# Kernel optimization log

Hardware: AMD Instinct MI355X
Metric: run time of the kernel (lower is better)

The kernel has to match this reference:

```python
import jax, jax.numpy as jnp
import numpy as np

B, T, D, H = 2, 2048, 1024, 16
DK = D // H
NEG = -1e9  # stand-in for -inf; causal mask guarantees >=1 valid key per row


def setup_inputs() -> dict:
    key = jax.random.key(0)
    ks = jax.random.split(key, 9)
    s = 1.0 / np.sqrt(D)
    x = jax.random.normal(ks[0], (B, T, D), dtype=jnp.float32)
    mask = jnp.broadcast_to(jnp.tril(jnp.ones((T, T), dtype=jnp.int32))[None, None], (B, 1, T, T))
    params = {}
    for i, n in enumerate(['q', 'k', 'v', 'o']):
        params['W' + n] = jax.random.normal(ks[1 + 2 * i], (D, D), dtype=jnp.float32) * s
        params['b' + n] = jax.random.normal(ks[2 + 2 * i], (D,), dtype=jnp.float32) * s
    return dict(x=x, mask=mask, **params)


def reference(x, mask, Wq, bq, Wk, bk, Wv, bv, Wo, bo):
    Bx, Tx, Dx = x.shape
    # projections: [B,T,D] -> [B,H,T,DK]
    def split_heads(y):
        return y.reshape(Bx, Tx, H, DK).transpose(0, 2, 1, 3)
    Q = split_heads(x @ Wq + bq)
    K = split_heads(x @ Wk + bk)
    V = split_heads(x @ Wv + bv)
    scores = jnp.einsum('bhqd,bhkd->bhqk', Q, K) / jnp.sqrt(jnp.float32(DK))
    scores = jnp.where(mask == 0, NEG, scores)
    attn = jax.nn.softmax(scores, axis=-1)  # dropout is identity in eval / p=0
    out = jnp.einsum('bhqk,bhkd->bhqd', attn, V)
    out = out.transpose(0, 2, 1, 3).reshape(Bx, Tx, Dx)
    return out @ Wo + bo
```

## Files before the change

kernel.cpp:

```cpp
#include <hip/hip_runtime.h>
#include <hip/hip_bf16.h>

typedef __bf16 bf16;
typedef __attribute__((ext_vector_type(8))) __bf16 bf16x8;
typedef __attribute__((ext_vector_type(4))) __bf16 bf16x4;
typedef __attribute__((ext_vector_type(4))) float f32x4;
typedef __attribute__((ext_vector_type(16))) float f32x16;
typedef __attribute__((ext_vector_type(4))) int int4v;

#define TSEQ 2048
#define DMODEL 1024
#define NHEAD 16
#define DKH 64
#define BATCH 2
#define NQKV 3072

typedef __attribute__((address_space(1))) const void gv_t;
typedef __attribute__((address_space(3))) void sv_t;
__device__ __forceinline__ void gll16(const bf16* g, bf16* s) {
    __builtin_amdgcn_global_load_lds((gv_t*)g, (sv_t*)s, 16, 0, 0);
}
#define WAIT_VM(n) __builtin_amdgcn_s_waitcnt(0x0F70 | (n))

__device__ __forceinline__ unsigned cvtpk(float lo, float hi) {
    unsigned d;
    asm("v_cvt_pk_bf16_f32 %0, %1, %2" : "=v"(d) : "v"(lo), "v"(hi));
    return d;
}

#define PREP_CONV 4096
#define PREP_TW   4096
#define PREP_GRID (PREP_CONV + PREP_TW + 12)
__global__ __launch_bounds__(256) void prep(
    const float* __restrict__ x,
    const float* __restrict__ Wq, const float* __restrict__ Wk,
    const float* __restrict__ Wv, const float* __restrict__ Wo,
    const float* __restrict__ bq, const float* __restrict__ bk,
    const float* __restrict__ bv,
    bf16* __restrict__ xb, bf16* __restrict__ WT, float* __restrict__ biasO)
{
    __shared__ float t[32][33];
    int bid = blockIdx.x;
    const int tid = threadIdx.x;
    if (bid < PREP_CONV) {
        int i = (bid * 256 + tid) * 4;
        f32x4 v = *(const f32x4*)(x + i);
        bf16x4 o;
#pragma unroll
        for (int j = 0; j < 4; ++j) o[j] = (bf16)v[j];
        *(bf16x4*)(xb + i) = o;
        return;
    }
    bid -= PREP_CONV;
    if (bid < PREP_TW) {
        int z = bid >> 10;
        int by = ((bid >> 5) & 31) * 32, bx = (bid & 31) * 32;
        const float* W = z == 0 ? Wq : z == 1 ? Wk : z == 2 ? Wv : Wo;
        bf16* T = WT + (size_t)z * DMODEL * DMODEL;
        int tx = tid & 31, ty = tid >> 5;
#pragma unroll
        for (int i = 0; i < 4; ++i)
            t[ty + i * 8][tx] = W[(size_t)(by + ty + i * 8) * DMODEL + bx + tx];
        __syncthreads();
#pragma unroll
        for (int i = 0; i < 4; ++i)
            T[(size_t)(bx + ty + i * 8) * DMODEL + by + tx] = (bf16)t[tx][ty + i * 8];
        return;
    }
    bid -= PREP_TW;
    int i = bid * 256 + tid;
    float v = i < 1024 ? bq[i] : i < 2048 ? bk[i - 1024] : bv[i - 2048];
    biasO[i] = v;
}

template <typename OutT, int NW_N, bool FUSE_VT>
__global__ __launch_bounds__(256) void gemm_bias_kernel(
    const bf16* __restrict__ A, const bf16* __restrict__ BT,
    const float* __restrict__ bias, OutT* __restrict__ C, int ldc,
    bf16* __restrict__ VT)
{
    constexpr int BN    = NW_N * 64;
    constexpr int MW    = 4 / NW_N;
    constexpr int WROWS = 128 / MW;
    constexpr int FM    = WROWS / 16;
    constexpr int BK    = 64;
    constexpr int ASZ   = 128 * BK;
    constexpr int BSZ   = BN * BK;
    constexpr int BNP   = BN + 4;
    constexpr int TST   = 136;
    constexpr int EPI   = sizeof(OutT) == 2 ? (FUSE_VT ? 128 * TST : 128 * BN)
                                            : 64 * BNP * 2;
    constexpr int STG   = 2 * ASZ + 2 * BSZ;
    constexpr int SMEM  = STG > EPI ? STG : EPI;
    __shared__ bf16 smem[SMEM];
    bf16* As0 = smem;
    bf16* Bs0 = smem + 2 * ASZ;

    const int tid = threadIdx.x;
    const int ln = tid & 63, wave = tid >> 6;
    const int wm = NW_N == 2 ? (wave >> 1) : wave;
    const int wn = NW_N == 2 ? (wave & 1) : 0;
    const int lr = ln & 15, quad = ln >> 4;

    constexpr int NBX = (NW_N == 2) ? 24 : 16;
    constexpr int CH  = (NW_N == 2) ? 96 : 64;
    const int wg  = blockIdx.x;
    const int lin = (wg & 7) * CH + (wg >> 3);
    const int m0  = (lin / NBX) * 128, n0 = (lin % NBX) * BN;

    f32x4 acc[FM][4] = {};

    const int srow = ln >> 3;
    const int scol = ((ln & 7) ^ srow) * 8;
    const bf16* Ag = A + (size_t)(m0 + wave * 32 + srow) * DMODEL + scol;
    const bf16* Bg = BT + (size_t)(n0 + (NW_N == 2 ? wave * 32 : wave * 16) + srow) * DMODEL + scol;

    auto stage = [&](int buf, int kk) {
        bf16* AsW = As0 + buf * ASZ + wave * (32 * BK);
#pragma unroll
        for (int l = 0; l < 4; ++l)
            gll16(Ag + (size_t)(l * 8) * DMODEL + kk, AsW + l * 8 * BK);
        if constexpr (NW_N == 2) {
            bf16* BsW = Bs0 + buf * BSZ + wave * (32 * BK);
#pragma unroll
            for (int l = 0; l < 4; ++l)
                gll16(Bg + (size_t)(l * 8) * DMODEL + kk, BsW + l * 8 * BK);
        } else {
            bf16* BsW = Bs0 + buf * BSZ + wave * (16 * BK);
#pragma unroll
            for (int l = 0; l < 2; ++l)
                gll16(Bg + (size_t)(l * 8) * DMODEL + kk, BsW + l * 8 * BK);
        }
    };

    constexpr int NT = DMODEL / BK;
    stage(0, 0);
    WAIT_VM(0);
    __syncthreads();
    const int swr = lr & 7;
    for (int kt = 0; kt < NT; ++kt) {
        if (kt + 1 < NT) stage((kt + 1) & 1, (kt + 1) * BK);
        const bf16* AsB = As0 + (kt & 1) * ASZ;
        const bf16* BsB = Bs0 + (kt & 1) * BSZ;
#pragma unroll
        for (int k2 = 0; k2 < 2; ++k2) {
            bf16x8 af[FM], bfr[4];
#pragma unroll
            for (int i = 0; i < FM; ++i)
                af[i] = *(const bf16x8*)(AsB + (wm * WROWS + i * 16 + lr) * BK +
                                         (((k2 * 4 + quad) ^ swr) * 8));
#pragma unroll
            for (int j = 0; j < 4; ++j)
                bfr[j] = *(const bf16x8*)(BsB + (wn * 64 + j * 16 + lr) * BK +
                                          (((k2 * 4 + quad) ^ swr) * 8));
#pragma unroll
            for (int i = 0; i < FM; ++i)
#pragma unroll
                for (int j = 0; j < 4; ++j)
                    acc[i][j] = __builtin_amdgcn_mfma_f32_16x16x32_bf16(
                        af[i], bfr[j], acc[i][j], 0, 0, 0);
        }
        WAIT_VM(0);
        __syncthreads();
    }

    if constexpr (sizeof(OutT) == 2) {
        if (FUSE_VT && n0 >= 2048) {
            bf16* Cs = smem;
#pragma unroll
            for (int j = 0; j < 4; ++j) {
                int nl = wn * 64 + j * 16 + lr;
                float bv = bias[n0 + nl];
#pragma unroll
                for (int i = 0; i < FM; ++i) {
                    int ml = wm * WROWS + i * 16 + quad * 4;
#pragma unroll
                    for (int r = 0; r < 4; ++r)
                        Cs[nl * TST + ml + r] = (bf16)(acc[i][j][r] + bv);
                }
            }
            __syncthreads();
            const int bb = m0 >> 11;
            const int tloc = m0 & 2047;
#pragma unroll
            for (int pp = 0; pp < 8; ++pp) {
                int dl = pp * 16 + (tid >> 4);
                int t0 = (tid & 15) * 8;
                bf16x8 v = *(const bf16x8*)(Cs + dl * TST + t0);
                *(bf16x8*)(VT + (size_t)(bb * 1024 + (n0 - 2048) + dl) * TSEQ +
                           tloc + t0) = v;
            }
            return;
        }
        bf16* Cs = smem;
#pragma unroll
        for (int j = 0; j < 4; ++j) {
            int nl = wn * 64 + j * 16 + lr;
            float bv = bias[n0 + nl];
#pragma unroll
            for (int i = 0; i < FM; ++i) {
                int ml = wm * WROWS + i * 16 + quad * 4;
#pragma unroll
                for (int r = 0; r < 4; ++r)
                    Cs[(ml + r) * BN + nl] = (bf16)(acc[i][j][r] + bv);
            }
        }
        __syncthreads();
        constexpr int LPR = BN / 8;
        constexpr int RPP = 256 / LPR;
        const int rr = tid / LPR, cc = (tid % LPR) * 8;
#pragma unroll
        for (int pp = 0; pp < 128 / RPP; ++pp) {
            int row = pp * RPP + rr;
            *(bf16x8*)(C + (size_t)(m0 + row) * ldc + n0 + cc) =
                *(const bf16x8*)(Cs + row * BN + cc);
        }
    } else {
        float* Cf = (float*)smem;
#pragma unroll
        for (int half = 0; half < 2; ++half) {
            if (((wm * WROWS) >> 6) == half) {
#pragma unroll
                for (int j = 0; j < 4; ++j) {
                    int nl = wn * 64 + j * 16 + lr;
                    float bv = bias[n0 + nl];
#pragma unroll
                    for (int i = 0; i < FM; ++i) {
                        int ml = wm * WROWS + i * 16 + quad * 4 - half * 64;
#pragma unroll
                        for (int r = 0; r < 4; ++r)
                            Cf[(ml + r) * BNP + nl] = acc[i][j][r] + bv;
                    }
                }
            }
            __syncthreads();
            constexpr int LPR = BN / 4;
            constexpr int RPP = 256 / LPR;
            const int rr = tid / LPR, cc = (tid % LPR) * 4;
#pragma unroll
            for (int pp = 0; pp < 64 / RPP; ++pp) {
                int row = pp * RPP + rr;
                *(f32x4*)(C + (size_t)(m0 + half * 64 + row) * ldc + n0 + cc) =
                    *(const f32x4*)(Cf + row * BNP + cc);
            }
            __syncthreads();
        }
    }
}

template <int KTN, bool MASKED>
__device__ __forceinline__ void tile_step(
    int kt0, int kc, int qabs,
    const bf16* __restrict__ Ksb, const bf16* __restrict__ Vsb,
    const bf16x8 qf[4], f32x16 oacc[2], float& lrow,
    int ln31, int hi, int sw)
{
    f32x16 st[KTN] = {};
    __builtin_amdgcn_s_setprio(1);
#pragma unroll
    for (int t = 0; t < KTN; ++t)
#pragma unroll
        for (int ks = 0; ks < 4; ++ks) {
            const bf16x8 ka = *(const bf16x8*)(
                Ksb + (ln31 + (kt0 + t) * 32) * 64 + (((2 * ks + hi) ^ sw) * 8));
            st[t] = __builtin_amdgcn_mfma_f32_32x32x16_bf16(ka, qf[ks], st[t], 0, 0, 0);
        }
    __builtin_amdgcn_s_setprio(0);

    const float scale2 = 0.18033688f;
    float rs = 0.f;
#pragma unroll
    for (int t = 0; t < KTN; ++t)
#pragma unroll
        for (int r = 0; r < 16; ++r) {
            float p = exp2f(fmaf(st[t][r], scale2, -24.0f));
            if (MASKED &&
                (kc + (kt0 + t) * 32 + (r & 3) + 8 * (r >> 2) + 4 * hi > qabs))
                p = 0.f;
            rs += p;
            st[t][r] = p;
        }
    rs += __shfl_xor(rs, 32);
    lrow += rs;

    __builtin_amdgcn_s_setprio(1);
#pragma unroll
    for (int t = 0; t < KTN; ++t)
#pragma unroll
        for (int s2 = 0; s2 < 2; ++s2) {
            const int bb = s2 * 8;
            unsigned c01 = cvtpk(st[t][bb + 0], st[t][bb + 1]);
            unsigned c23 = cvtpk(st[t][bb + 2], st[t][bb + 3]);
            unsigned c45 = cvtpk(st[t][bb + 4], st[t][bb + 5]);
            unsigned c67 = cvtpk(st[t][bb + 6], st[t][bb + 7]);
            asm("v_permlane32_swap_b32 %0, %1" : "+v"(c01), "+v"(c45));
            asm("v_permlane32_swap_b32 %0, %1" : "+v"(c23), "+v"(c67));
            int4v pw;
            pw[0] = (int)c01; pw[1] = (int)c23; pw[2] = (int)c45; pw[3] = (int)c67;
            const bf16x8 pa = __builtin_bit_cast(bf16x8, pw);
            const int ksg = (kt0 + t) * 2 + s2;
#pragma unroll
            for (int dblk = 0; dblk < 2; ++dblk) {
                const bf16x8 vb = *(const bf16x8*)(
                    Vsb + (dblk * 32 + ln31) * 64 + (((2 * ksg + hi) ^ sw) * 8));
                oacc[dblk] = __builtin_amdgcn_mfma_f32_32x32x16_bf16(
                    pa, vb, oacc[dblk], 0, 0, 0);
            }
        }
    __builtin_amdgcn_s_setprio(0);
}

__global__ __launch_bounds__(256, 2) void flash_attn(
    const bf16* __restrict__ QKV, const bf16* __restrict__ VT,
    bf16* __restrict__ O)
{
    __shared__ bf16 Ks[4][64 * 64];
    __shared__ bf16 Vs[4][64 * 64];
    const int tid = threadIdx.x;
    const int ln = tid & 63, w = tid >> 6;
    const int ln31 = ln & 31, hi = ln >> 5, sw = ln & 7;
    const int wg = blockIdx.x;
    const int g = wg & 31, p = wg >> 5;
    const int h = g >> 1, b = g & 1;
    const int q0A = p * 64, q0B = (31 - p) * 64;

    const bf16* Qb = QKV + (size_t)b * TSEQ * NQKV + h * DKH;
    const bf16* Kb = Qb + 1024;
    const bf16* VTb = VT + (size_t)(b * NHEAD + h) * DKH * TSEQ;

    const int q1 = (w < 2 ? q0A : q0B) + (w & 1) * 32 + ln31;
    const int q2 = q0B + (w & 1) * 32 + ln31;

    bf16x8 qf1[4], qf2[4];
#pragma unroll
    for (int ks = 0; ks < 4; ++ks) {
        qf1[ks] = *(const bf16x8*)(Qb + (size_t)q1 * NQKV + ks * 16 + hi * 8);
        qf2[ks] = *(const bf16x8*)(Qb + (size_t)q2 * NQKV + ks * 16 + hi * 8);
    }
    WAIT_VM(0);

    const int srow = (w & 1) * 32 + (ln >> 3);
    const int scol = ((ln & 7) ^ ((ln >> 3) & 7)) * 8;
    const bool stK = (w < 2);
    auto stage = [&](int buf, int kc) {
        if (stK) {
            const bf16* g2 = Kb + (size_t)(kc + srow) * NQKV + scol;
            bf16* s = &Ks[buf][(w & 1) * 32 * 64];
#pragma unroll
            for (int l = 0; l < 4; ++l)
                gll16(g2 + (size_t)(l * 8) * NQKV, s + l * 8 * 64);
        } else {
            const bf16* g2 = VTb + (size_t)srow * TSEQ + kc + scol;
            bf16* s = &Vs[buf][(w & 1) * 32 * 64];
#pragma unroll
            for (int l = 0; l < 4; ++l)
                gll16(g2 + (size_t)(l * 8) * TSEQ, s + l * 8 * 64);
        }
    };

    f32x16 oacc1[2] = {}, oacc2[2] = {};
    float l1 = 0.f, l2 = 0.f;

    const int nld = 32 - p;

    auto do_chunk = [&](int c) {
        const int kc = c * 64;
        const bf16* K = Ks[c & 3];
        const bf16* V = Vs[c & 3];
        if (c <= p) {
            if (w < 2 && c == p)
                tile_step<2, true >(0, kc, q1, K, V, qf1, oacc1, l1, ln31, hi, sw);
            else
                tile_step<2, false>(0, kc, q1, K, V, qf1, oacc1, l1, ln31, hi, sw);
        } else {
            const int kt0 = w >> 1;
            if (c == nld - 1)
                tile_step<1, true >(kt0, kc, q2, K, V, qf2, oacc2, l2, ln31, hi, sw);
            else
                tile_step<1, false>(kt0, kc, q2, K, V, qf2, oacc2, l2, ln31, hi, sw);
        }
    };

    stage(0, 0);
    stage(1, 64);
    for (int c = 0; c < nld; c += 2) {
        WAIT_VM(0);
        __syncthreads();
        if (c + 2 < nld) stage((c + 2) & 3, (c + 2) * 64);
        if (c + 3 < nld) stage((c + 3) & 3, (c + 3) * 64);
        do_chunk(c);
        if (c + 1 < nld) do_chunk(c + 1);
    }
    __syncthreads();

    float* exO = (float*)&Ks[0][0];
    float* exL = (float*)&Vs[0][0];
    if (w < 2) {
        float* dst = exO + w * 2048;
#pragma unroll
        for (int dblk = 0; dblk < 2; ++dblk)
#pragma unroll
            for (int r = 0; r < 16; ++r) {
                int q = (r & 3) + 8 * (r >> 2) + 4 * hi;
                dst[q * 64 + dblk * 32 + ln31] = oacc2[dblk][r];
            }
        if (ln < 32) exL[w * 32 + ln] = l2;
    }
    __syncthreads();

    f32x16 oat[2];
    float lt;
    int qs;
    if (w < 2) {
        oat[0] = oacc1[0]; oat[1] = oacc1[1];
        lt = l1;
        qs = q0A + (w & 1) * 32;
    } else {
        const float* src = exO + (w - 2) * 2048;
        lt = l1 + l2 + exL[(w - 2) * 32 + ln31];
#pragma unroll
        for (int dblk = 0; dblk < 2; ++dblk)
#pragma unroll
            for (int r = 0; r < 16; ++r) {
                int q = (r & 3) + 8 * (r >> 2) + 4 * hi;
                oat[dblk][r] = oacc1[dblk][r] + oacc2[dblk][r] +
                               src[q * 64 + dblk * 32 + ln31];
            }
        qs = q0B + (w & 1) * 32;
    }

#pragma unroll
    for (int r = 0; r < 16; ++r) {
        const int crow = (r & 3) + 8 * (r >> 2) + 4 * hi;
        const float inv = 1.0f / __shfl(lt, crow);
        const int row = qs + crow;
#pragma unroll
        for (int dblk = 0; dblk < 2; ++dblk)
            O[(size_t)(b * TSEQ + row) * DMODEL + h * DKH + dblk * 32 + ln31] =
                (bf16)(oat[dblk][r] * inv);
    }
}

extern "C" void kernel_launch(void* const* d_in, const int* in_sizes, int n_in,
                              void* d_out, int out_size, void* d_ws, size_t ws_size,
                              hipStream_t stream)
{
    const float* x  = (const float*)d_in[0];
    const float* Wq = (const float*)d_in[2];
    const float* bq = (const float*)d_in[3];
    const float* Wk = (const float*)d_in[4];
    const float* bk = (const float*)d_in[5];
    const float* Wv = (const float*)d_in[6];
    const float* bv = (const float*)d_in[7];
    const float* Wo = (const float*)d_in[8];
    const float* bo = (const float*)d_in[9];

    char* ws = (char*)d_ws;
    bf16* xb   = (bf16*)(ws);
    bf16* QKV  = (bf16*)(ws + (8u  << 20));
    bf16* VT   = (bf16*)(ws + (32u << 20));
    bf16* O    = (bf16*)(ws + (40u << 20));
    bf16* WT   = (bf16*)(ws + (48u << 20));
    float* wsBias = (float*)O;

    prep<<<PREP_GRID, 256, 0, stream>>>(x, Wq, Wk, Wv, Wo, bq, bk, bv,
                                        xb, WT, wsBias);

    gemm_bias_kernel<bf16, 2, true><<<768, 256, 0, stream>>>(
        xb, WT, wsBias, QKV, NQKV, VT);

    flash_attn<<<512, 256, 0, stream>>>(QKV, VT, O);

    gemm_bias_kernel<float, 1, false><<<512, 256, 0, stream>>>(
        O, WT + 3u * (1u << 20), bo, (float*)d_out, DMODEL, nullptr);
}
```

Measured before the change: 198.7 us.

## Split attention key range across two workgroups and merge with combine kernel

Each attention work item is split into two workgroups. They take alternating 64-key chunks and write unnormalized bf16 partial outputs plus row sums to workspace. A new combine kernel adds the two partials and divides by the summed normalizer. LDS staging shrinks from four buffers to two so occupancy can rise to four workgroups per CU, and the QK buffer row stride drops to 2048. The goal is more parallelism and better latency hiding, at the cost of an extra launch, extra partial-output traffic, and bf16 rounding of unnormalized partials.

After: 269.0 us. 35.4% more time.

```diff
diff --git a/kernel.cpp b/kernel.cpp
--- a/kernel.cpp
+++ b/kernel.cpp
@@ -14,6 +14,7 @@
 #define DKH 64
 #define BATCH 2
 #define NQKV 3072
+#define QKROW 2048
 
 typedef __attribute__((address_space(1))) const void gv_t;
 typedef __attribute__((address_space(3))) void sv_t;
@@ -310,21 +311,23 @@
     __builtin_amdgcn_s_setprio(0);
 }
 
-__global__ __launch_bounds__(256, 2) void flash_attn(
-    const bf16* __restrict__ QKV, const bf16* __restrict__ VT,
-    bf16* __restrict__ O)
+__global__ __launch_bounds__(256, 4) void flash_attn(
+    const bf16* __restrict__ QK, const bf16* __restrict__ VT,
+    bf16* __restrict__ Op0, bf16* __restrict__ Op1, float* __restrict__ lpart)
 {
-    __shared__ bf16 Ks[4][64 * 64];
-    __shared__ bf16 Vs[4][64 * 64];
+    __shared__ bf16 Ks[2][64 * 64];
+    __shared__ bf16 Vs[2][64 * 64];
     const int tid = threadIdx.x;
     const int ln = tid & 63, w = tid >> 6;
     const int ln31 = ln & 31, hi = ln >> 5, sw = ln & 7;
     const int wg = blockIdx.x;
-    const int g = wg & 31, p = wg >> 5;
+    const int g = wg & 31;
+    const int p = (wg >> 5) & 15;
+    const int half = wg >> 9;
     const int h = g >> 1, b = g & 1;
     const int q0A = p * 64, q0B = (31 - p) * 64;
 
-    const bf16* Qb = QKV + (size_t)b * TSEQ * NQKV + h * DKH;
+    const bf16* Qb = QK + (size_t)b * TSEQ * QKROW + h * DKH;
     const bf16* Kb = Qb + 1024;
     const bf16* VTb = VT + (size_t)(b * NHEAD + h) * DKH * TSEQ;
 
@@ -334,8 +337,8 @@
     bf16x8 qf1[4], qf2[4];
 #pragma unroll
     for (int ks = 0; ks < 4; ++ks) {
-        qf1[ks] = *(const bf16x8*)(Qb + (size_t)q1 * NQKV + ks * 16 + hi * 8);
-        qf2[ks] = *(const bf16x8*)(Qb + (size_t)q2 * NQKV + ks * 16 + hi * 8);
+        qf1[ks] = *(const bf16x8*)(Qb + (size_t)q1 * QKROW + ks * 16 + hi * 8);
+        qf2[ks] = *(const bf16x8*)(Qb + (size_t)q2 * QKROW + ks * 16 + hi * 8);
     }
     WAIT_VM(0);
 
@@ -344,11 +347,11 @@
     const bool stK = (w < 2);
     auto stage = [&](int buf, int kc) {
         if (stK) {
-            const bf16* g2 = Kb + (size_t)(kc + srow) * NQKV + scol;
+            const bf16* g2 = Kb + (size_t)(kc + srow) * QKROW + scol;
             bf16* s = &Ks[buf][(w & 1) * 32 * 64];
 #pragma unroll
             for (int l = 0; l < 4; ++l)
-                gll16(g2 + (size_t)(l * 8) * NQKV, s + l * 8 * 64);
+                gll16(g2 + (size_t)(l * 8) * QKROW, s + l * 8 * 64);
         } else {
             const bf16* g2 = VTb + (size_t)srow * TSEQ + kc + scol;
             bf16* s = &Vs[buf][(w & 1) * 32 * 64];
@@ -362,11 +365,12 @@
     float l1 = 0.f, l2 = 0.f;
 
     const int nld = 32 - p;
-
-    auto do_chunk = [&](int c) {
+    const int ni = (nld - half + 1) >> 1;
+
+    auto do_chunk = [&](int c, int buf) {
         const int kc = c * 64;
-        const bf16* K = Ks[c & 3];
-        const bf16* V = Vs[c & 3];
+        const bf16* K = Ks[buf];
+        const bf16* V = Vs[buf];
         if (c <= p) {
             if (w < 2 && c == p)
                 tile_step<2, true >(0, kc, q1, K, V, qf1, oacc1, l1, ln31, hi, sw);
@@ -381,17 +385,15 @@
         }
     };
 
-    stage(0, 0);
-    stage(1, 64);
-    for (int c = 0; c < nld; c += 2) {
+    stage(0, half * 64);
+    WAIT_VM(0);
+    __syncthreads();
+    for (int i = 0; i < ni; ++i) {
+        if (i + 1 < ni) stage((i + 1) & 1, (half + 2 * (i + 1)) * 64);
+        do_chunk(half + 2 * i, i & 1);
         WAIT_VM(0);
         __syncthreads();
-        if (c + 2 < nld) stage((c + 2) & 3, (c + 2) * 64);
-        if (c + 3 < nld) stage((c + 3) & 3, (c + 3) * 64);
-        do_chunk(c);
-        if (c + 1 < nld) do_chunk(c + 1);
-    }
-    __syncthreads();
+    }
 
     float* exO = (float*)&Ks[0][0];
     float* exL = (float*)&Vs[0][0];
@@ -429,16 +431,40 @@
         qs = q0B + (w & 1) * 32;
     }
 
+    bf16* Ob = (b == 0 ? Op0 : Op1) + (size_t)half * (TSEQ * DMODEL);
+    float* lp = lpart + half * 65536 + b * 32768 + h * 2048;
+    if (hi == 0) lp[qs + ln31] = lt;
 #pragma unroll
     for (int r = 0; r < 16; ++r) {
         const int crow = (r & 3) + 8 * (r >> 2) + 4 * hi;
-        const float inv = 1.0f / __shfl(lt, crow);
         const int row = qs + crow;
 #pragma unroll
         for (int dblk = 0; dblk < 2; ++dblk)
-            O[(size_t)(b * TSEQ + row) * DMODEL + h * DKH + dblk * 32 + ln31] =
-                (bf16)(oat[dblk][r] * inv);
-    }
+            Ob[(size_t)row * DMODEL + h * DKH + dblk * 32 + ln31] =
+                (bf16)oat[dblk][r];
+    }
+}
+
+__global__ __launch_bounds__(256) void combine(
+    const bf16* __restrict__ Op0, const bf16* __restrict__ Op1,
+    const float* __restrict__ lpart, bf16* __restrict__ O)
+{
+    const int i = blockIdx.x * 256 + threadIdx.x;
+    const size_t e = (size_t)i * 8;
+    const int b = (int)(e >> 21);
+    const int rem = (int)(e & ((1u << 21) - 1));
+    const int row = rem >> 10, hd = rem & 1023, h = hd >> 6;
+    const bf16* base = (b == 0 ? Op0 : Op1);
+    bf16x8 p0 = *(const bf16x8*)(base + rem);
+    bf16x8 p1 = *(const bf16x8*)(base + (1u << 21) + rem);
+    const float l = lpart[b * 32768 + h * 2048 + row] +
+                    lpart[65536 + b * 32768 + h * 2048 + row];
+    const float inv = 1.0f / l;
+    bf16x8 o;
+#pragma unroll
+    for (int j = 0; j < 8; ++j)
+        o[j] = (bf16)((float(p0[j]) + float(p1[j])) * inv);
+    *(bf16x8*)(O + e) = o;
 }
 
 extern "C" void kernel_launch(void* const* d_in, const int* in_sizes, int n_in,
@@ -456,20 +482,25 @@
     const float* bo = (const float*)d_in[9];
 
     char* ws = (char*)d_ws;
-    bf16* xb   = (bf16*)(ws);
-    bf16* QKV  = (bf16*)(ws + (8u  << 20));
-    bf16* VT   = (bf16*)(ws + (32u << 20));
-    bf16* O    = (bf16*)(ws + (40u << 20));
-    bf16* WT   = (bf16*)(ws + (48u << 20));
+    bf16* xb    = (bf16*)(ws);
+    bf16* QK    = (bf16*)(ws + (8u  << 20));
+    bf16* VT    = (bf16*)(ws + (24u << 20));
+    bf16* Op1   = (bf16*)(ws + (32u << 20));
+    bf16* O     = (bf16*)(ws + (40u << 20));
+    bf16* WT    = (bf16*)(ws + (48u << 20));
     float* wsBias = (float*)O;
+    float* lpart  = (float*)WT;
+    bf16* Op0   = xb;
 
     prep<<<PREP_GRID, 256, 0, stream>>>(x, Wq, Wk, Wv, Wo, bq, bk, bv,
                                         xb, WT, wsBias);
 
     gemm_bias_kernel<bf16, 2, true><<<768, 256, 0, stream>>>(
-        xb, WT, wsBias, QKV, NQKV, VT);
-
-    flash_attn<<<512, 256, 0, stream>>>(QKV, VT, O);
+        xb, WT, wsBias, QK, QKROW, VT);
+
+    flash_attn<<<1024, 256, 0, stream>>>(QK, VT, Op0, Op1, lpart);
+
+    combine<<<2048, 256, 0, stream>>>(Op0, Op1, lpart, O);
 
     gemm_bias_kernel<float, 1, false><<<512, 256, 0, stream>>>(
         O, WT + 3u * (1u << 20), bo, (float*)d_out, DMODEL, nullptr);
```

## Split flash attention into 1024 two-wave blocks with 32-row paired query tiles

Applied to the files above, without the earlier changes.

Restructures the attention kernel from 256-thread blocks owning two 64-row query tiles to 128-thread blocks owning two 32-row tiles (paired causally for load balance), doubling the grid to 1024 blocks. The K/V LDS ring shrinks from 4 to 2 buffers, with single-chunk double buffering and a barrier every chunk instead of every two chunks. The aim is more blocks and finer-grained work to improve occupancy and tail balance across CUs. In exchange each K/V tile is loaded by more blocks, which adds global/L2 traffic, and there are more barriers per unit of work.

After: 213.7 us. 7.5% more time.

```diff
diff --git a/kernel.cpp b/kernel.cpp
--- a/kernel.cpp
+++ b/kernel.cpp
@@ -310,26 +310,28 @@
     __builtin_amdgcn_s_setprio(0);
 }
 
-__global__ __launch_bounds__(256, 2) void flash_attn(
+__global__ __launch_bounds__(128, 2) void flash_attn(
     const bf16* __restrict__ QKV, const bf16* __restrict__ VT,
     bf16* __restrict__ O)
 {
-    __shared__ bf16 Ks[4][64 * 64];
-    __shared__ bf16 Vs[4][64 * 64];
+    __shared__ bf16 Ks[2][64 * 64];
+    __shared__ bf16 Vs[2][64 * 64];
     const int tid = threadIdx.x;
     const int ln = tid & 63, w = tid >> 6;
     const int ln31 = ln & 31, hi = ln >> 5, sw = ln & 7;
     const int wg = blockIdx.x;
-    const int g = wg & 31, p = wg >> 5;
+    const int g = wg & 31, P = wg >> 5;
     const int h = g >> 1, b = g & 1;
-    const int q0A = p * 64, q0B = (31 - p) * 64;
+    const int cA = P >> 1;
+    const int nld = ((63 - P) >> 1) + 1;
+    const int q0A = P * 32, q0B = (63 - P) * 32;
 
     const bf16* Qb = QKV + (size_t)b * TSEQ * NQKV + h * DKH;
     const bf16* Kb = Qb + 1024;
     const bf16* VTb = VT + (size_t)(b * NHEAD + h) * DKH * TSEQ;
 
-    const int q1 = (w < 2 ? q0A : q0B) + (w & 1) * 32 + ln31;
-    const int q2 = q0B + (w & 1) * 32 + ln31;
+    const int q1 = (w == 0 ? q0A : q0B) + ln31;
+    const int q2 = q0B + ln31;
 
     bf16x8 qf1[4], qf2[4];
 #pragma unroll
@@ -339,21 +341,20 @@
     }
     WAIT_VM(0);
 
-    const int srow = (w & 1) * 32 + (ln >> 3);
-    const int scol = ((ln & 7) ^ ((ln >> 3) & 7)) * 8;
-    const bool stK = (w < 2);
+    const int srow = ln >> 3;
+    const int scol = ((ln & 7) ^ srow) * 8;
     auto stage = [&](int buf, int kc) {
-        if (stK) {
+        if (w == 0) {
             const bf16* g2 = Kb + (size_t)(kc + srow) * NQKV + scol;
-            bf16* s = &Ks[buf][(w & 1) * 32 * 64];
-#pragma unroll
-            for (int l = 0; l < 4; ++l)
+            bf16* s = &Ks[buf][0];
+#pragma unroll
+            for (int l = 0; l < 8; ++l)
                 gll16(g2 + (size_t)(l * 8) * NQKV, s + l * 8 * 64);
         } else {
             const bf16* g2 = VTb + (size_t)srow * TSEQ + kc + scol;
-            bf16* s = &Vs[buf][(w & 1) * 32 * 64];
-#pragma unroll
-            for (int l = 0; l < 4; ++l)
+            bf16* s = &Vs[buf][0];
+#pragma unroll
+            for (int l = 0; l < 8; ++l)
                 gll16(g2 + (size_t)(l * 8) * TSEQ, s + l * 8 * 64);
         }
     };
@@ -361,72 +362,61 @@
     f32x16 oacc1[2] = {}, oacc2[2] = {};
     float l1 = 0.f, l2 = 0.f;
 
-    const int nld = 32 - p;
-
-    auto do_chunk = [&](int c) {
+    stage(0, 0);
+    WAIT_VM(0);
+    __syncthreads();
+    for (int c = 0; c < nld; ++c) {
+        if (c + 1 < nld) stage((c + 1) & 1, (c + 1) * 64);
         const int kc = c * 64;
-        const bf16* K = Ks[c & 3];
-        const bf16* V = Vs[c & 3];
-        if (c <= p) {
-            if (w < 2 && c == p)
+        const bf16* K = Ks[c & 1];
+        const bf16* V = Vs[c & 1];
+        if (c <= cA) {
+            if (w == 0 && c == cA)
                 tile_step<2, true >(0, kc, q1, K, V, qf1, oacc1, l1, ln31, hi, sw);
             else
                 tile_step<2, false>(0, kc, q1, K, V, qf1, oacc1, l1, ln31, hi, sw);
         } else {
-            const int kt0 = w >> 1;
             if (c == nld - 1)
-                tile_step<1, true >(kt0, kc, q2, K, V, qf2, oacc2, l2, ln31, hi, sw);
+                tile_step<1, true >(w, kc, q2, K, V, qf2, oacc2, l2, ln31, hi, sw);
             else
-                tile_step<1, false>(kt0, kc, q2, K, V, qf2, oacc2, l2, ln31, hi, sw);
-        }
-    };
-
-    stage(0, 0);
-    stage(1, 64);
-    for (int c = 0; c < nld; c += 2) {
+                tile_step<1, false>(w, kc, q2, K, V, qf2, oacc2, l2, ln31, hi, sw);
+        }
         WAIT_VM(0);
         __syncthreads();
-        if (c + 2 < nld) stage((c + 2) & 3, (c + 2) * 64);
-        if (c + 3 < nld) stage((c + 3) & 3, (c + 3) * 64);
-        do_chunk(c);
-        if (c + 1 < nld) do_chunk(c + 1);
-    }
-    __syncthreads();
+    }
 
     float* exO = (float*)&Ks[0][0];
     float* exL = (float*)&Vs[0][0];
-    if (w < 2) {
-        float* dst = exO + w * 2048;
+    if (w == 0) {
 #pragma unroll
         for (int dblk = 0; dblk < 2; ++dblk)
 #pragma unroll
             for (int r = 0; r < 16; ++r) {
                 int q = (r & 3) + 8 * (r >> 2) + 4 * hi;
-                dst[q * 64 + dblk * 32 + ln31] = oacc2[dblk][r];
-            }
-        if (ln < 32) exL[w * 32 + ln] = l2;
+                exO[q * 64 + dblk * 32 + ln31] = oacc2[dblk][r];
+            }
+        if (ln < 32) exL[ln] = l2;
     }
     __syncthreads();
 
     f32x16 oat[2];
     float lt;
     int qs;
-    if (w < 2) {
+    if (w == 0) {
         oat[0] = oacc1[0]; oat[1] = oacc1[1];
         lt = l1;
-        qs = q0A + (w & 1) * 32;
+        qs = q0A;
     } else {
-        const float* src = exO + (w - 2) * 2048;
-        lt = l1 + l2 + exL[(w - 2) * 32 + ln31];
+        lt = l1 + l2 + exL[ln31];
 #pragma unroll
         for (int dblk = 0; dblk < 2; ++dblk)
 #pragma unroll
             for (int r = 0; r < 16; ++r) {
                 int q = (r & 3) + 8 * (r >> 2) + 4 * hi;
                 oat[dblk][r] = oacc1[dblk][r] + oacc2[dblk][r] +
-                               src[q * 64 + dblk * 32 + ln31];
-            }
-        qs = q0B + (w & 1) * 32;
+                               exO[q * 64 + dblk * 32 + ln31];
+            }
+        qs = q0B;
     }
 
 #pragma unroll
@@ -469,7 +459,7 @@
     gemm_bias_kernel<bf16, 2, true><<<768, 256, 0, stream>>>(
         xb, WT, wsBias, QKV, NQKV, VT);
 
-    flash_attn<<<512, 256, 0, stream>>>(QKV, VT, O);
+    flash_attn<<<1024, 128, 0, stream>>>(QKV, VT, O);
 
     gemm_bias_kernel<float, 1, false><<<512, 256, 0, stream>>>(
         O, WT + 3u * (1u << 20), bo, (float*)d_out, DMODEL, nullptr);
```

## Split flash-attention KV chunks across two wave groups in 512-thread blocks

Applied to the files above, without the earlier changes.

The attention kernel now launches 512 threads per block: two groups of four waves each take alternating KV chunks, each group staging its own chunk into the shared ring buffers. The partial output accumulators and row sums from the two groups are merged through shared memory in a multi-stage reduction before normalization and the store. This roughly doubles the waves available to hide latency for each query tile. In exchange it adds a cross-group reduction with extra barriers, and the launch bound now asks for four 512-thread blocks per CU, which tightens the register budget and could cause spills.

New measurement: 256.4 us. +29.0%, slower.

```diff
diff --git a/kernel.cpp b/kernel.cpp
--- a/kernel.cpp
+++ b/kernel.cpp
@@ -310,7 +310,7 @@
     __builtin_amdgcn_s_setprio(0);
 }
 
-__global__ __launch_bounds__(256, 2) void flash_attn(
+__global__ __launch_bounds__(512, 4) void flash_attn(
     const bf16* __restrict__ QKV, const bf16* __restrict__ VT,
     bf16* __restrict__ O)
 {
@@ -318,6 +318,7 @@
     __shared__ bf16 Vs[4][64 * 64];
     const int tid = threadIdx.x;
     const int ln = tid & 63, w = tid >> 6;
+    const int grp = w >> 2, wl = w & 3;
     const int ln31 = ln & 31, hi = ln >> 5, sw = ln & 7;
     const int wg = blockIdx.x;
     const int g = wg & 31, p = wg >> 5;
@@ -328,8 +329,8 @@
     const bf16* Kb = Qb + 1024;
     const bf16* VTb = VT + (size_t)(b * NHEAD + h) * DKH * TSEQ;
 
-    const int q1 = (w < 2 ? q0A : q0B) + (w & 1) * 32 + ln31;
-    const int q2 = q0B + (w & 1) * 32 + ln31;
+    const int q1 = (wl < 2 ? q0A : q0B) + (wl & 1) * 32 + ln31;
+    const int q2 = q0B + (wl & 1) * 32 + ln31;
 
     bf16x8 qf1[4], qf2[4];
 #pragma unroll
@@ -339,19 +340,19 @@
     }
     WAIT_VM(0);
 
-    const int srow = (w & 1) * 32 + (ln >> 3);
+    const int srow = (wl & 1) * 32 + (ln >> 3);
     const int scol = ((ln & 7) ^ ((ln >> 3) & 7)) * 8;
-    const bool stK = (w < 2);
+    const bool stK = (wl < 2);
     auto stage = [&](int buf, int kc) {
         if (stK) {
             const bf16* g2 = Kb + (size_t)(kc + srow) * NQKV + scol;
-            bf16* s = &Ks[buf][(w & 1) * 32 * 64];
+            bf16* s = &Ks[buf][(wl & 1) * 32 * 64];
 #pragma unroll
             for (int l = 0; l < 4; ++l)
                 gll16(g2 + (size_t)(l * 8) * NQKV, s + l * 8 * 64);
         } else {
             const bf16* g2 = VTb + (size_t)srow * TSEQ + kc + scol;
-            bf16* s = &Vs[buf][(w & 1) * 32 * 64];
+            bf16* s = &Vs[buf][(wl & 1) * 32 * 64];
 #pragma unroll
             for (int l = 0; l < 4; ++l)
                 gll16(g2 + (size_t)(l * 8) * TSEQ, s + l * 8 * 64);
@@ -368,12 +369,12 @@
         const bf16* K = Ks[c & 3];
         const bf16* V = Vs[c & 3];
         if (c <= p) {
-            if (w < 2 && c == p)
+            if (wl < 2 && c == p)
                 tile_step<2, true >(0, kc, q1, K, V, qf1, oacc1, l1, ln31, hi, sw);
             else
                 tile_step<2, false>(0, kc, q1, K, V, qf1, oacc1, l1, ln31, hi, sw);
         } else {
-            const int kt0 = w >> 1;
+            const int kt0 = wl >> 1;
             if (c == nld - 1)
                 tile_step<1, true >(kt0, kc, q2, K, V, qf2, oacc2, l2, ln31, hi, sw);
             else
@@ -381,63 +382,109 @@
         }
     };
 
-    stage(0, 0);
-    stage(1, 64);
-    for (int c = 0; c < nld; c += 2) {
+    if (grp == 0) stage(0, 0);
+    else          stage(1, 64);
+    for (int c0 = 0; c0 < nld; c0 += 2) {
+        const int c = c0 + grp;
         WAIT_VM(0);
         __syncthreads();
-        if (c + 2 < nld) stage((c + 2) & 3, (c + 2) * 64);
-        if (c + 3 < nld) stage((c + 3) & 3, (c + 3) * 64);
-        do_chunk(c);
-        if (c + 1 < nld) do_chunk(c + 1);
-    }
+        const int cn = c + 2;
+        if (cn < nld) stage(cn & 3, cn * 64);
+        if (c < nld) do_chunk(c);
+    }
+    WAIT_VM(0);
     __syncthreads();
 
-    float* exO = (float*)&Ks[0][0];
-    float* exL = (float*)&Vs[0][0];
-    if (w < 2) {
-        float* dst = exO + w * 2048;
-#pragma unroll
-        for (int dblk = 0; dblk < 2; ++dblk)
+    float* base = (float*)&Ks[0][0];
+    float* AO  = base;
+    float* BO  = base + 4096;
+    float* BO2 = (float*)&Vs[0][0];
+    float* AL  = (float*)&Vs[2][0];
+    float* BL  = AL + 64;
+    float* BL2 = AL + 128;
+    const int rg = wl & 1;
+
+    if (grp == 1) {
+        if (wl < 2) {
+            float* dA = AO + rg * 2048;
+            float* dB = BO2 + rg * 2048;
+#pragma unroll
+            for (int dblk = 0; dblk < 2; ++dblk)
+#pragma unroll
+                for (int r = 0; r < 16; ++r) {
+                    int q = (r & 3) + 8 * (r >> 2) + 4 * hi;
+                    dA[q * 64 + dblk * 32 + ln31] = oacc1[dblk][r];
+                    dB[q * 64 + dblk * 32 + ln31] = oacc2[dblk][r];
+                }
+            if (ln < 32) { AL[rg * 32 + ln] = l1; BL2[rg * 32 + ln] = l2; }
+        } else {
+            float* dB = BO + rg * 2048;
+#pragma unroll
+            for (int dblk = 0; dblk < 2; ++dblk)
+#pragma unroll
+                for (int r = 0; r < 16; ++r) {
+                    int q = (r & 3) + 8 * (r >> 2) + 4 * hi;
+                    dB[q * 64 + dblk * 32 + ln31] = oacc1[dblk][r] + oacc2[dblk][r];
+                }
+            if (ln < 32) BL[rg * 32 + ln] = l1 + l2;
+        }
+    }
+    __syncthreads();
+    if (grp == 0) {
+        if (wl < 2) {
+            float* dB = BO2 + rg * 2048;
+#pragma unroll
+            for (int dblk = 0; dblk < 2; ++dblk)
+#pragma unroll
+                for (int r = 0; r < 16; ++r) {
+                    int q = (r & 3) + 8 * (r >> 2) + 4 * hi;
+                    dB[q * 64 + dblk * 32 + ln31] += oacc2[dblk][r];
+                }
+            if (ln < 32) BL2[rg * 32 + ln] += l2;
+            const float* sA = AO + rg * 2048;
+            float lt = l1 + AL[rg * 32 + ln31];
+            const int qs = q0A + rg * 32;
 #pragma unroll
             for (int r = 0; r < 16; ++r) {
-                int q = (r & 3) + 8 * (r >> 2) + 4 * hi;
-                dst[q * 64 + dblk * 32 + ln31] = oacc2[dblk][r];
-            }
-        if (ln < 32) exL[w * 32 + ln] = l2;
+                const int crow = (r & 3) + 8 * (r >> 2) + 4 * hi;
+                const float inv = 1.0f / __shfl(lt, crow);
+                const int row = qs + crow;
+#pragma unroll
+                for (int dblk = 0; dblk < 2; ++dblk)
+                    O[(size_t)(b * TSEQ + row) * DMODEL + h * DKH + dblk * 32 + ln31] =
+                        (bf16)((oacc1[dblk][r] +
+                                sA[crow * 64 + dblk * 32 + ln31]) * inv);
+            }
+        } else {
+            float* dB = BO + rg * 2048;
+#pragma unroll
+            for (int dblk = 0; dblk < 2; ++dblk)
+#pragma unroll
+                for (int r = 0; r < 16; ++r) {
+                    int q = (r & 3) + 8 * (r >> 2) + 4 * hi;
+                    dB[q * 64 + dblk * 32 + ln31] += oacc1[dblk][r] + oacc2[dblk][r];
+                }
+            if (ln < 32) BL[rg * 32 + ln] += l1 + l2;
+        }
     }
     __syncthreads();
-
-    f32x16 oat[2];
-    float lt;
-    int qs;
-    if (w < 2) {
-        oat[0] = oacc1[0]; oat[1] = oacc1[1];
-        lt = l1;
-        qs = q0A + (w & 1) * 32;
-    } else {
-        const float* src = exO + (w - 2) * 2048;
-        lt = l1 + l2 + exL[(w - 2) * 32 + ln31];
-#pragma unroll
-        for (int dblk = 0; dblk < 2; ++dblk)
-#pragma unroll
-            for (int r = 0; r < 16; ++r) {
-                int q = (r & 3) + 8 * (r >> 2) + 4 * hi;
-                oat[dblk][r] = oacc1[dblk][r] + oacc2[dblk][r] +
-                               src[q * 64 + dblk * 32 + ln31];
-            }
-        qs = q0B + (w & 1) * 32;
-    }
-
-#pragma unroll
-    for (int r = 0; r < 16; ++r) {
-        const int crow = (r & 3) + 8 * (r >> 2) + 4 * hi;
-        const float inv = 1.0f / __shfl(lt, crow);
-        const int row = qs + crow;
-#pragma unroll
-        for (int dblk = 0; dblk < 2; ++dblk)
-            O[(size_t)(b * TSEQ + row) * DMODEL + h * DKH + dblk * 32 + ln31] =
-                (bf16)(oat[dblk][r] * inv);
+    if (grp == 0 && wl >= 2) {
+        const float* sB  = BO + rg * 2048;
+        const float* sB2 = BO2 + rg * 2048;
+        float lt = BL[rg * 32 + ln31] + BL2[rg * 32 + ln31];
+        const int qs = q0B + rg * 32;
+#pragma unroll
+        for (int r = 0; r < 16; ++r) {
+            const int crow = (r & 3) + 8 * (r >> 2) + 4 * hi;
+            const float inv = 1.0f / __shfl(lt, crow);
+            const int row = qs + crow;
+#pragma unroll
+            for (int dblk = 0; dblk < 2; ++dblk) {
+                const int idx = crow * 64 + dblk * 32 + ln31;
+                O[(size_t)(b * TSEQ + row) * DMODEL + h * DKH + dblk * 32 + ln31] =
+                    (bf16)((sB[idx] + sB2[idx]) * inv);
+            }
+        }
     }
 }
 
@@ -469,7 +516,7 @@
     gemm_bias_kernel<bf16, 2, true><<<768, 256, 0, stream>>>(
         xb, WT, wsBias, QKV, NQKV, VT);
 
-    flash_attn<<<512, 256, 0, stream>>>(QKV, VT, O);
+    flash_attn<<<512, 512, 0, stream>>>(QKV, VT, O);
 
     gemm_bias_kernel<float, 1, false><<<512, 256, 0, stream>>>(
         O, WT + 3u * (1u << 20), bo, (float*)d_out, DMODEL, nullptr);
```
